# Performance work log

Measured on AMD Instinct MI355X. Metric: run time of the kernel, lower is better.

Reference implementation:

```python
import jax, jax.numpy as jnp
import numpy as np
from jax import lax

V, EMB, ENH, DNH, ZD, K = 51, 64, 256, 256, 32, 512
B, T = 1024, 128


def gru_scan(xs, h0, Wih, Whh, bih, bhh, collect):
    """PyTorch-convention GRU. xs: [T,B,D], h0: [B,H]. Returns (ys or None, hT)."""
    def step(h, x):
        gi = x @ Wih.T + bih          # [B, 3H]
        gh = h @ Whh.T + bhh          # [B, 3H]
        ir, iz, inn = jnp.split(gi, 3, axis=-1)
        hr, hz, hn = jnp.split(gh, 3, axis=-1)
        r = jax.nn.sigmoid(ir + hr)
        zg = jax.nn.sigmoid(iz + hz)
        n = jnp.tanh(inn + r * hn)
        hnew = (1.0 - zg) * n + zg * h
        return hnew, (hnew if collect else None)
    hT, ys = lax.scan(step, h0, xs)
    return ys, hT


def setup_inputs() -> dict:
    key = jax.random.key(0)
    ks = jax.random.split(key, 24)
    w = lambda k, shape, s=0.1: (jax.random.normal(k, shape, jnp.float32) * s)
    inp = {
        "x": jax.random.randint(ks[0], (B, T), 0, V),
        "emb_enc": w(ks[1], (V, EMB)),
        "emb_dec": w(ks[2], (V, EMB)),
        # encoder bidirectional GRU (fwd + bwd directions)
        "Wih_f": w(ks[3], (3 * ENH, EMB)), "Whh_f": w(ks[4], (3 * ENH, ENH)),
        "bih_f": w(ks[5], (3 * ENH,)), "bhh_f": w(ks[6], (3 * ENH,)),
        "Wih_b": w(ks[7], (3 * ENH, EMB)), "Whh_b": w(ks[8], (3 * ENH, ENH)),
        "bih_b": w(ks[9], (3 * ENH,)), "bhh_b": w(ks[10], (3 * ENH,)),
        # down_to_z: Linear(2*ENC_NH -> Z_NH)
        "Wdown": w(ks[11], (ZD, 2 * ENH)), "bdown": w(ks[12], (ZD,)),
        # VQ codebook, uniform(-1/K, 1/K) as in source
        "codebook": jax.random.uniform(ks[13], (K, ZD), jnp.float32, -1.0 / K, 1.0 / K),
        # up_from_z: Linear(Z_NH -> DEC_NH)
        "Wup": w(ks[14], (DNH, ZD)), "bup": w(ks[15], (DNH,)),
        # decoder GRU: input = INPUT_EMB_DIM + Z_NH
        "Wih_d": w(ks[16], (3 * DNH, EMB + ZD)), "Whh_d": w(ks[17], (3 * DNH, DNH)),
        "bih_d": w(ks[18], (3 * DNH,)), "bhh_d": w(ks[19], (3 * DNH,)),
        # output projection Linear(DEC_NH -> VOCABSIZE)
        "Wout": w(ks[20], (V, DNH)), "bout": w(ks[21], (V,)),
    }
    return inp


def reference(x, emb_enc, emb_dec, Wih_f, Whh_f, bih_f, bhh_f,
              Wih_b, Whh_b, bih_b, bhh_b, Wdown, bdown, codebook,
              Wup, bup, Wih_d, Whh_d, bih_d, bhh_d, Wout, bout):
    sg = lax.stop_gradient
    Bsz, Tlen = x.shape

    # ---- Encoder: bidirectional GRU, keep final hidden of each direction ----
    e = emb_enc[x]                              # [B,T,EMB]
    xs = jnp.transpose(e, (1, 0, 2))            # [T,B,EMB]
    h0 = jnp.zeros((Bsz, ENH), e.dtype)
    _, hf = gru_scan(xs, h0, Wih_f, Whh_f, bih_f, bhh_f, collect=False)
    _, hb = gru_scan(xs[::-1], h0, Wih_b, Whh_b, bih_b, bhh_b, collect=False)
    out_h = jnp.concatenate([hf, hb], axis=-1)  # [B, 2*ENH]

    # ---- down to z ----
    z = out_h @ Wdown.T + bdown                 # [B, ZD]

    # ---- VQ quantizer ----
    d2 = (z ** 2).sum(-1, keepdims=True) + (codebook ** 2).sum(-1) - 2.0 * (z @ codebook.T)  # [B,K]
    idx = jnp.argmin(d2, axis=-1)               # [B]
    quantized = codebook[idx]                   # [B, ZD]
    commit = ((sg(quantized) - z) ** 2).mean(-1)
    embed_l = ((quantized - sg(z)) ** 2).mean(-1)
    qloss = 0.1 * commit + 0.1 * embed_l
    Q = jnp.sum(qloss)
    qz = z + sg(quantized - z)                  # straight-through [B, ZD]

    # ---- up to decoder hidden ----
    hidden = qz @ Wup.T + bup                   # [B, DNH]

    # ---- Decoder GRU over src, z concatenated at every step ----
    src, tgt = x[:, :-1], x[:, 1:]
    d = emb_dec[src]                            # [B,T-1,EMB]
    zrep = jnp.broadcast_to(qz[:, None, :], (Bsz, Tlen - 1, ZD))
    dec_in = jnp.concatenate([zrep, d], axis=-1)            # [B,T-1,EMB+ZD]
    ys, _ = gru_scan(jnp.transpose(dec_in, (1, 0, 2)), hidden,
                     Wih_d, Whh_d, bih_d, bhh_d, collect=True)  # [T-1,B,DNH]
    logits = jnp.transpose(ys, (1, 0, 2)) @ Wout.T + bout   # [B,T-1,V]

    # cross entropy, reduction='sum', ignore_index=0
    logp = jax.nn.log_softmax(logits, axis=-1)
    nll = -jnp.take_along_axis(logp, tgt[..., None], axis=-1).squeeze(-1)  # [B,T-1]
    mask = (tgt != 0)
    xloss = jnp.sum(nll * mask)
    nonpadded_tokens = jnp.sum(mask)
    pred_tokens = jnp.argmax(logits, axis=-1)

    return (xloss, nonpadded_tokens, pred_tokens, Q, idx[:, None])
```

## Files before the change

kernel.cpp:

```cpp
#include <hip/hip_runtime.h>
#include <cstdint>

typedef unsigned short u16;
typedef unsigned int u32;
typedef __attribute__((ext_vector_type(4))) int int4v;
typedef __attribute__((ext_vector_type(8))) short short8;
typedef __attribute__((ext_vector_type(4))) float f32x4;

#define XLOSS_OFF 0
#define NPAD_OFF  1
#define PRED_OFF  2
#define Q_OFF     130050
#define IDX_OFF   130051

__device__ __forceinline__ u16 f2b(float f){
  union { float f; unsigned int i; } c; c.f = f;
  unsigned int i = c.i;
  unsigned int r = (i + 0x7FFFu + ((i >> 16) & 1u)) >> 16;
  return (u16)r;
}

#define LOG2E 1.442695040889634f
__device__ __forceinline__ float fast_sigmoid(float x){
  return __builtin_amdgcn_rcpf(1.f + __builtin_amdgcn_exp2f(-LOG2E*x));
}
__device__ __forceinline__ float fast_tanh(float x){
  return 1.f - 2.f*__builtin_amdgcn_rcpf(1.f + __builtin_amdgcn_exp2f((2.f*LOG2E)*x));
}

__global__ __launch_bounds__(256) void k_prep_wo(
    const float* __restrict__ Wo, u16* __restrict__ oWo, float* __restrict__ dout){
  int idx = blockIdx.x*256 + threadIdx.x;
  if (idx == 0){ dout[XLOSS_OFF]=0.f; dout[NPAD_OFF]=0.f; dout[Q_OFF]=0.f; }
  int row = idx >> 8, k = idx & 255;
  oWo[idx] = (row < 51) ? f2b(Wo[row*256 + k]) : (u16)0;
}

__global__ __launch_bounds__(64) void k_prep_q(
    const float* __restrict__ Wf, const float* __restrict__ Wb, const float* __restrict__ Wd,
    signed char* __restrict__ qf, signed char* __restrict__ qb, signed char* __restrict__ qd,
    float* __restrict__ invf, float* __restrict__ invb, float* __restrict__ invd){
  const int row = blockIdx.x;
  const int mat = row / 768, r = row - mat*768;
  const float* W = (mat==0 ? Wf : (mat==1 ? Wb : Wd)) + (size_t)r*256;
  signed char* q = (mat==0 ? qf : (mat==1 ? qb : qd)) + (size_t)r*256;
  float* inv     = (mat==0 ? invf : (mat==1 ? invb : invd));
  const int lane = threadIdx.x;
  float4 v = *(const float4*)(W + lane*4);
  float m = fmaxf(fmaxf(fabsf(v.x),fabsf(v.y)), fmaxf(fabsf(v.z),fabsf(v.w)));
  #pragma unroll
  for (int off=32; off>0; off>>=1) m = fmaxf(m, __shfl_xor(m, off));
  m = fmaxf(m, 1e-20f);
  const float s = 127.f / m;
  int a0 = __float2int_rn(v.x*s), a1 = __float2int_rn(v.y*s);
  int a2 = __float2int_rn(v.z*s), a3 = __float2int_rn(v.w*s);
  u32 packed = (a0&255) | ((a1&255)<<8) | ((a2&255)<<16) | ((a3&255)<<24);
  *(u32*)(q + lane*4) = packed;
  if (lane == 0) inv[r] = m * (1.f/127.f);
}

__global__ __launch_bounds__(256) void k_prep_g(
    const float* __restrict__ emb_e, const float* __restrict__ emb_d,
    const float* __restrict__ Wih_f, const float* __restrict__ bih_f, const float* __restrict__ bhh_f,
    const float* __restrict__ Wih_b, const float* __restrict__ bih_b, const float* __restrict__ bhh_b,
    const float* __restrict__ Wih_d,
    float* __restrict__ Gf, float* __restrict__ Gb, float* __restrict__ Gd){
  int idx = blockIdx.x*256 + threadIdx.x;
  int tab = idx / 39168;
  int rem = idx - tab*39168;
  int v = rem / 768;
  int n = rem - v*768;
  float acc = 0.f;
  if (tab == 0){
    const float* e = emb_e + v*64; const float* w = Wih_f + n*64;
    for (int k=0;k<64;k++) acc += e[k]*w[k];
    acc += bih_f[n] + (n < 512 ? bhh_f[n] : 0.f);
    Gf[rem] = acc;
  } else if (tab == 1){
    const float* e = emb_e + v*64; const float* w = Wih_b + n*64;
    for (int k=0;k<64;k++) acc += e[k]*w[k];
    acc += bih_b[n] + (n < 512 ? bhh_b[n] : 0.f);
    Gb[rem] = acc;
  } else {
    const float* e = emb_d + v*64; const float* w = Wih_d + n*96 + 32;
    for (int k=0;k<64;k++) acc += e[k]*w[k];
    Gd[rem] = acc;
  }
}

template<int MODE>
__global__ __launch_bounds__(512)
__attribute__((amdgpu_waves_per_eu(2, 2)))
void k_gru(
    const signed char* __restrict__ W0, const signed char* __restrict__ W1,
    const float* __restrict__ I0, const float* __restrict__ I1,
    const float* __restrict__ G0, const float* __restrict__ G1,
    const float* __restrict__ bhh0, const float* __restrict__ bhh1,
    const int* __restrict__ x,
    const float* __restrict__ zc, const float* __restrict__ h0g,
    float* __restrict__ out_h, u16* __restrict__ ys){
  __shared__ signed char hbf[2*4096];
  __shared__ int xsh[2048];

  const int tid = threadIdx.x;
  const int lane = tid & 63;
  const int wave = tid >> 6;
  const int l15 = lane & 15, lhi = lane >> 4;

  bool fwd = true; int gb;
  const signed char* W; const float* G; const float* bhh; const float* invS;
  if (MODE == 0){
    int bi = blockIdx.x;
    fwd = bi < 64; gb = fwd ? bi : bi - 64;
    W = fwd ? W0 : W1; G = fwd ? G0 : G1; bhh = fwd ? bhh0 : bhh1;
    invS = fwd ? I0 : I1;
  } else {
    gb = blockIdx.x; W = W0; G = G0; bhh = bhh0; invS = I0;
  }
  const int b0 = gb * 16;
  const int nT = (MODE == 0) ? 128 : 127;
  const float HS    = (MODE == 0) ? 127.f : 63.f;
  const float invHS = (MODE == 0) ? (1.f/127.f) : (1.f/63.f);

  const int ca  = wave*32 + l15;
  const int cb2 = ca + 16;

  int4v wq[6][4];
  #pragma unroll
  for (int g=0; g<3; g++){
    #pragma unroll
    for (int hh=0; hh<2; hh++){
      const signed char* p = W + (size_t)(g*256 + wave*32 + hh*16 + l15)*256 + lhi*16;
      #pragma unroll
      for (int kt=0; kt<4; kt++)
        wq[g*2+hh][kt] = *(const int4v*)(p + kt*64);
    }
  }
  #pragma unroll
  for (int kt=0; kt<4; kt++){
    asm volatile("" : "+v"(wq[0][kt]));
    asm volatile("" : "+v"(wq[1][kt]));
    asm volatile("" : "+v"(wq[2][kt]));
    asm volatile("" : "+v"(wq[3][kt]));
    asm volatile("" : "+v"(wq[4][kt]));
    asm volatile("" : "+v"(wq[5][kt]));
  }
  const float is0 = invS[ca]        * invHS;
  const float is1 = invS[cb2]       * invHS;
  const float is2 = invS[256 + ca]  * invHS;
  const float is3 = invS[256 + cb2] * invHS;
  const float is4 = invS[512 + ca]  * invHS;
  const float is5 = invS[512 + cb2] * invHS;
  const float bn0 = bhh[512 + ca];
  const float bn1 = bhh[512 + cb2];

  for (int i = tid; i < 2048; i += 512) xsh[i] = x[b0*128 + i];

  float hr0[4], hr1[4];
  #pragma unroll
  for (int r=0;r<4;r++){
    const int m = 4*lhi + r;
    const int sw = (m&15)<<4;
    float v0 = (MODE==0) ? 0.f : h0g[(size_t)(b0+m)*256 + ca];
    float v1 = (MODE==0) ? 0.f : h0g[(size_t)(b0+m)*256 + cb2];
    hr0[r] = v0; hr1[r] = v1;
    int q0 = __float2int_rn(fminf(fmaxf(v0*HS, -127.f), 127.f));
    int q1 = __float2int_rn(fminf(fmaxf(v1*HS, -127.f), 127.f));
    hbf[m*256 + (ca  ^ sw)] = (signed char)q0;
    hbf[m*256 + (cb2 ^ sw)] = (signed char)q1;
  }
  __syncthreads();

  int aoff[4];
  #pragma unroll
  for (int kt=0; kt<4; kt++)
    aoff[kt] = l15*256 + ((kt*64 + lhi*16) ^ (l15<<4));

  int cur = 0;
  for (int t=0; t<nT; ++t){
    const signed char* hb = hbf + (cur<<12);
    int4v af[4];
    #pragma unroll
    for (int kt=0; kt<4; kt++) af[kt] = *(const int4v*)(hb + aoff[kt]);

    int4v acc[6];
    #pragma unroll
    for (int j=0;j<6;j++) acc[j] = (int4v){0,0,0,0};
    #pragma unroll
    for (int kt=0; kt<4; kt++)
      #pragma unroll
      for (int j=0;j<6;j++)
        acc[j] = __builtin_amdgcn_mfma_i32_16x16x64_i8(af[kt], wq[j][kt], acc[j], 0,0,0);

    const int te = (MODE==0 && !fwd) ? (127 - t) : t;
    signed char* nbuf = hbf + ((cur^1)<<12);
    #pragma unroll
    for (int r=0;r<4;r++){
      const int m = 4*lhi + r;
      const int tok = xsh[(m<<7) + te];
      const float* Gp = G + (size_t)tok*768;
      float gr0 = Gp[ca],  gz0 = Gp[256+ca],  gn0 = Gp[512+ca];
      float gr1 = Gp[cb2], gz1 = Gp[256+cb2], gn1 = Gp[512+cb2];
      if (MODE==1){
        const float* zp = zc + (size_t)(b0+m)*768;
        gr0 += zp[ca];  gz0 += zp[256+ca];  gn0 += zp[512+ca];
        gr1 += zp[cb2]; gz1 += zp[256+cb2]; gn1 += zp[512+cb2];
      }
      const int sw = (m&15)<<4;
      {
        float rg = fast_sigmoid((float)acc[0][r]*is0 + gr0);
        float zg = fast_sigmoid((float)acc[2][r]*is2 + gz0);
        float nn = fast_tanh(gn0 + rg*((float)acc[4][r]*is4 + bn0));
        float hv = nn + zg*(hr0[r] - nn);
        hr0[r] = hv;
        int hq = __float2int_rn(fminf(fmaxf(hv*HS, -127.f), 127.f));
        nbuf[m*256 + (ca ^ sw)] = (signed char)hq;
        if (MODE == 1) ys[((size_t)(b0+m)*127 + t)*256 + ca] = f2b(hv);
      }
      {
        float rg = fast_sigmoid((float)acc[1][r]*is1 + gr1);
        float zg = fast_sigmoid((float)acc[3][r]*is3 + gz1);
        float nn = fast_tanh(gn1 + rg*((float)acc[5][r]*is5 + bn1));
        float hv = nn + zg*(hr1[r] - nn);
        hr1[r] = hv;
        int hq = __float2int_rn(fminf(fmaxf(hv*HS, -127.f), 127.f));
        nbuf[m*256 + (cb2 ^ sw)] = (signed char)hq;
        if (MODE == 1) ys[((size_t)(b0+m)*127 + t)*256 + cb2] = f2b(hv);
      }
    }
    __syncthreads();
    cur ^= 1;
  }

  if (MODE == 0){
    #pragma unroll
    for (int r=0;r<4;r++){
      const int m = 4*lhi + r;
      float* dst = out_h + (size_t)(b0+m)*512 + (fwd ? 0 : 256);
      dst[ca]  = hr0[r];
      dst[cb2] = hr1[r];
    }
  }
}

__global__ __launch_bounds__(64) void k_vq(
    const float* __restrict__ outH, const float* __restrict__ Wdown, const float* __restrict__ bdown,
    const float* __restrict__ cb, const float* __restrict__ Wup, const float* __restrict__ bup,
    const float* __restrict__ Wihd, const float* __restrict__ bihd, const float* __restrict__ bhhd,
    float* __restrict__ hidden, float* __restrict__ zc, float* __restrict__ dout){
  const int b = blockIdx.x;
  const int lane = threadIdx.x;
  __shared__ float oh[512];
  __shared__ float zsh[32];
  __shared__ float qsh[32];
  {
    const float* src = outH + (size_t)b*512 + lane*8;
    *(float4*)&oh[lane*8]   = *(const float4*)src;
    *(float4*)&oh[lane*8+4] = *(const float4*)(src+4);
  }
  __syncthreads();
  if (lane < 32){
    float acc = bdown[lane];
    const float* wr = Wdown + lane*512;
    for (int k=0;k<512;k++) acc += wr[k]*oh[k];
    zsh[lane] = acc;
  }
  __syncthreads();
  float bd = 3.4e38f; int bi = 0;
  for (int c8=0;c8<8;c8++){
    const int c = lane*8 + c8;
    const float* cr = cb + c*32;
    float d = 0.f;
    #pragma unroll
    for (int k=0;k<32;k++){ float df = zsh[k]-cr[k]; d += df*df; }
    if (d < bd){ bd = d; bi = c; }
  }
  #pragma unroll
  for (int offm=32; offm>0; offm>>=1){
    float od = __shfl_xor(bd, offm);
    int   oi = __shfl_xor(bi, offm);
    if (od < bd || (od == bd && oi < bi)){ bd = od; bi = oi; }
  }
  if (lane == 0){
    atomicAdd(&dout[Q_OFF], bd * (0.2f/32.f));
    dout[IDX_OFF + b] = (float)bi;
  }
  if (lane < 32) qsh[lane] = cb[(size_t)bi*32 + lane];
  __syncthreads();
  #pragma unroll
  for (int i=0;i<4;i++){
    const int o = lane*4 + i;
    float acc = bup[o];
    const float* wr = Wup + o*32;
    #pragma unroll
    for (int k=0;k<32;k++) acc += wr[k]*qsh[k];
    hidden[(size_t)b*256 + o] = acc;
  }
  #pragma unroll
  for (int i=0;i<12;i++){
    const int o = lane*12 + i;
    float acc = bihd[o] + (o < 512 ? bhhd[o] : 0.f);
    const float* wr = Wihd + (size_t)o*96;
    #pragma unroll
    for (int k=0;k<32;k++) acc += wr[k]*qsh[k];
    zc[(size_t)b*768 + o] = acc;
  }
}

__global__ __launch_bounds__(256) void k_out(
    const u16* __restrict__ ys, const u16* __restrict__ Wo,
    const float* __restrict__ bout, const int* __restrict__ x,
    float* __restrict__ dout){
  const int tid = threadIdx.x;
  const int w = tid >> 6, lane = tid & 63;
  const int l15 = lane & 15, lhi = lane >> 4;
  __shared__ float lg[4][32][66];
  const int rows0 = blockIdx.x*128 + w*32;
  const f32x4 fz = {0.f,0.f,0.f,0.f};
  #pragma unroll
  for (int mt=0; mt<2; mt++){
    const int rb = rows0 + mt*16;
    f32x4 acc[4];
    #pragma unroll
    for (int nt=0;nt<4;nt++) acc[nt] = fz;
    #pragma unroll
    for (int kt=0; kt<8; kt++){
      short8 a = *(const short8*)&ys[(size_t)(rb + l15)*256 + kt*32 + lhi*8];
      #pragma unroll
      for (int nt=0; nt<4; nt++){
        short8 bb = *(const short8*)&Wo[(size_t)(nt*16 + l15)*256 + kt*32 + lhi*8];
        acc[nt] = __builtin_amdgcn_mfma_f32_16x16x32_bf16(a, bb, acc[nt], 0, 0, 0);
      }
    }
    #pragma unroll
    for (int nt=0;nt<4;nt++){
      const int col = nt*16 + l15;
      const float bo = (col < 51) ? bout[col] : 0.f;
      #pragma unroll
      for (int r=0;r<4;r++){
        float v = (col < 51) ? (acc[nt][r] + bo) : -1e30f;
        lg[w][mt*16 + lhi*4 + r][col] = v;
      }
    }
  }
  __syncthreads();
  float xl = 0.f, ct = 0.f;
  if (lane < 32){
    const int grow = rows0 + lane;
    const float* Lr = &lg[w][lane][0];
    float m = Lr[0]; int am = 0;
    for (int i=1;i<51;i++){ float v = Lr[i]; if (v > m){ m = v; am = i; } }
    float s = 0.f;
    for (int i=0;i<51;i++) s += __expf(Lr[i] - m);
    const int bb = grow / 127;
    const int tt = grow - bb*127;
    const int tgt = x[bb*128 + tt + 1];
    const float nll = (m + __logf(s)) - Lr[tgt];
    const float mk = (tgt != 0) ? 1.f : 0.f;
    dout[PRED_OFF + grow] = (float)am;
    xl = nll * mk; ct = mk;
  }
  #pragma unroll
  for (int off=32; off>0; off>>=1){
    xl += __shfl_xor(xl, off);
    ct += __shfl_xor(ct, off);
  }
  if (lane == 0){
    atomicAdd(&dout[XLOSS_OFF], xl);
    atomicAdd(&dout[NPAD_OFF], ct);
  }
}

extern "C" void kernel_launch(void* const* d_in, const int* in_sizes, int n_in,
                              void* d_out, int out_size, void* d_ws, size_t ws_size,
                              hipStream_t stream){
  (void)in_sizes; (void)n_in; (void)out_size; (void)ws_size;
  const int*   x      = (const int*)  d_in[0];
  const float* emb_e  = (const float*)d_in[1];
  const float* emb_d  = (const float*)d_in[2];
  const float* Wih_f  = (const float*)d_in[3];
  const float* Whh_f  = (const float*)d_in[4];
  const float* bih_f  = (const float*)d_in[5];
  const float* bhh_f  = (const float*)d_in[6];
  const float* Wih_b  = (const float*)d_in[7];
  const float* Whh_b  = (const float*)d_in[8];
  const float* bih_b  = (const float*)d_in[9];
  const float* bhh_b  = (const float*)d_in[10];
  const float* Wdown  = (const float*)d_in[11];
  const float* bdown  = (const float*)d_in[12];
  const float* cbook  = (const float*)d_in[13];
  const float* Wup    = (const float*)d_in[14];
  const float* bup    = (const float*)d_in[15];
  const float* Wih_d  = (const float*)d_in[16];
  const float* Whh_d  = (const float*)d_in[17];
  const float* bih_d  = (const float*)d_in[18];
  const float* bhh_d  = (const float*)d_in[19];
  const float* Wout   = (const float*)d_in[20];
  const float* bout   = (const float*)d_in[21];
  float* dout = (float*)d_out;

  char* ws = (char*)d_ws;
  size_t off = 0;
  auto nxt = [&](size_t bytes)->char*{
    char* r = ws + off;
    off += (bytes + 255) & ~(size_t)255;
    return r;
  };
  signed char* Wq_f = (signed char*)nxt((size_t)196608);
  signed char* Wq_b = (signed char*)nxt((size_t)196608);
  signed char* Wq_d = (signed char*)nxt((size_t)196608);
  float* invF = (float*)nxt((size_t)768*4);
  float* invB = (float*)nxt((size_t)768*4);
  float* invD = (float*)nxt((size_t)768*4);
  float* Gf    = (float*)nxt((size_t)39168*4);
  float* Gb    = (float*)nxt((size_t)39168*4);
  float* Gd    = (float*)nxt((size_t)39168*4);
  u16*   Wo_bf = (u16*) nxt((size_t)16384*2);
  float* outH  = (float*)nxt((size_t)524288*4);
  float* hid   = (float*)nxt((size_t)262144*4);
  float* zcw   = (float*)nxt((size_t)786432*4);
  u16*   ysb   = (u16*)  nxt((size_t)33292288*2);

  hipLaunchKernelGGL(k_prep_wo, dim3(64), dim3(256), 0, stream, Wout, Wo_bf, dout);
  hipLaunchKernelGGL(k_prep_q, dim3(2304), dim3(64), 0, stream,
                     Whh_f, Whh_b, Whh_d, Wq_f, Wq_b, Wq_d, invF, invB, invD);
  hipLaunchKernelGGL(k_prep_g, dim3(459), dim3(256), 0, stream,
                     emb_e, emb_d, Wih_f, bih_f, bhh_f, Wih_b, bih_b, bhh_b, Wih_d,
                     Gf, Gb, Gd);
  hipLaunchKernelGGL((k_gru<0>), dim3(128), dim3(512), 0, stream,
                     Wq_f, Wq_b, invF, invB, Gf, Gb, bhh_f, bhh_b, x,
                     (const float*)nullptr, (const float*)nullptr, outH, (u16*)nullptr);
  hipLaunchKernelGGL(k_vq, dim3(1024), dim3(64), 0, stream,
                     outH, Wdown, bdown, cbook, Wup, bup, Wih_d, bih_d, bhh_d,
                     hid, zcw, dout);
  hipLaunchKernelGGL((k_gru<1>), dim3(64), dim3(512), 0, stream,
                     Wq_d, (const signed char*)nullptr, invD, (const float*)nullptr,
                     Gd, (const float*)nullptr, bhh_d, (const float*)nullptr, x,
                     zcw, hid, (float*)nullptr, ysb);
  hipLaunchKernelGGL(k_out, dim3(1016), dim3(256), 0, stream,
                     ysb, Wo_bf, bout, x, dout);
}
```

Baseline: 601.3 us.

## Halve GRU batch per block and redistribute gate math via LDS

Each GRU block now handles 8 batch rows instead of 16, doubling the grid so more CUs take part in the sequential recurrence. The MFMA tiles still compute 16 rows, so half the work is padding. Accumulators are staged through shared memory, letting each wave handle one batch row with vectorised 4-wide gate math, packed int8 and bf16 stores, and a zc tile cached in LDS. The token-dependent G loads are issued before the MFMAs. In exchange each timestep gets an extra barrier and more LDS traffic.

```diff
diff --git a/kernel.cpp b/kernel.cpp
--- a/kernel.cpp
+++ b/kernel.cpp
@@ -100,7 +100,9 @@
     const float* __restrict__ zc, const float* __restrict__ h0g,
     float* __restrict__ out_h, u16* __restrict__ ys){
   __shared__ signed char hbf[2*4096];
-  __shared__ int xsh[2048];
+  __shared__ int xsh[1024];
+  __shared__ int gh[8*772];
+  __shared__ float zcs[(MODE==1) ? 8*768 : 4];
 
   const int tid = threadIdx.x;
   const int lane = tid & 63;
@@ -111,19 +113,16 @@
   const signed char* W; const float* G; const float* bhh; const float* invS;
   if (MODE == 0){
     int bi = blockIdx.x;
-    fwd = bi < 64; gb = fwd ? bi : bi - 64;
+    fwd = bi < 128; gb = fwd ? bi : bi - 128;
     W = fwd ? W0 : W1; G = fwd ? G0 : G1; bhh = fwd ? bhh0 : bhh1;
     invS = fwd ? I0 : I1;
   } else {
     gb = blockIdx.x; W = W0; G = G0; bhh = bhh0; invS = I0;
   }
-  const int b0 = gb * 16;
+  const int b0 = gb * 8;
   const int nT = (MODE == 0) ? 128 : 127;
   const float HS    = (MODE == 0) ? 127.f : 63.f;
   const float invHS = (MODE == 0) ? (1.f/127.f) : (1.f/63.f);
-
-  const int ca  = wave*32 + l15;
-  const int cb2 = ca + 16;
 
   int4v wq[6][4];
   #pragma unroll
@@ -145,29 +144,38 @@
     asm volatile("" : "+v"(wq[4][kt]));
     asm volatile("" : "+v"(wq[5][kt]));
   }
-  const float is0 = invS[ca]        * invHS;
-  const float is1 = invS[cb2]       * invHS;
-  const float is2 = invS[256 + ca]  * invHS;
-  const float is3 = invS[256 + cb2] * invHS;
-  const float is4 = invS[512 + ca]  * invHS;
-  const float is5 = invS[512 + cb2] * invHS;
-  const float bn0 = bhh[512 + ca];
-  const float bn1 = bhh[512 + cb2];
-
-  for (int i = tid; i < 2048; i += 512) xsh[i] = x[b0*128 + i];
-
-  float hr0[4], hr1[4];
-  #pragma unroll
-  for (int r=0;r<4;r++){
-    const int m = 4*lhi + r;
-    const int sw = (m&15)<<4;
-    float v0 = (MODE==0) ? 0.f : h0g[(size_t)(b0+m)*256 + ca];
-    float v1 = (MODE==0) ? 0.f : h0g[(size_t)(b0+m)*256 + cb2];
-    hr0[r] = v0; hr1[r] = v1;
-    int q0 = __float2int_rn(fminf(fmaxf(v0*HS, -127.f), 127.f));
-    int q1 = __float2int_rn(fminf(fmaxf(v1*HS, -127.f), 127.f));
-    hbf[m*256 + (ca  ^ sw)] = (signed char)q0;
-    hbf[m*256 + (cb2 ^ sw)] = (signed char)q1;
+
+  const int gm = wave;
+  const int c4 = lane * 4;
+  f32x4 isr4 = *(const f32x4*)(invS + c4);
+  f32x4 isz4 = *(const f32x4*)(invS + 256 + c4);
+  f32x4 isn4 = *(const f32x4*)(invS + 512 + c4);
+  #pragma unroll
+  for (int i=0;i<4;i++){ isr4[i] *= invHS; isz4[i] *= invHS; isn4[i] *= invHS; }
+  const f32x4 bn4 = *(const f32x4*)(bhh + 512 + c4);
+
+  for (int i = tid; i < 1024; i += 512) xsh[i] = x[b0*128 + i];
+  for (int i = tid*4; i < 8192; i += 2048) *(int*)&hbf[i] = 0;
+  if (MODE == 1){
+    const f32x4* src = (const f32x4*)(zc + (size_t)b0*768);
+    f32x4* dst = (f32x4*)zcs;
+    for (int i = tid; i < 1536; i += 512) dst[i] = src[i];
+  }
+  __syncthreads();
+
+  float hreg[4];
+  #pragma unroll
+  for (int i=0;i<4;i++) hreg[i] = 0.f;
+  if (MODE == 1){
+    f32x4 h0v = *(const f32x4*)(h0g + (size_t)(b0+gm)*256 + c4);
+    u32 pk = 0;
+    #pragma unroll
+    for (int i=0;i<4;i++){
+      hreg[i] = h0v[i];
+      int q = __float2int_rn(fminf(fmaxf(h0v[i]*HS, -127.f), 127.f));
+      pk |= (u32)(q & 255) << (8*i);
+    }
+    *(u32*)&hbf[gm*256 + (c4 ^ (gm<<4))] = pk;
   }
   __syncthreads();
 
@@ -178,6 +186,13 @@
 
   int cur = 0;
   for (int t=0; t<nT; ++t){
+    const int te = (MODE==0 && !fwd) ? (127 - t) : t;
+    const int tok = xsh[(gm<<7) + te];
+    const float* Gp = G + (size_t)tok*768 + c4;
+    f32x4 gr4 = *(const f32x4*)(Gp);
+    f32x4 gz4 = *(const f32x4*)(Gp + 256);
+    f32x4 gn4 = *(const f32x4*)(Gp + 512);
+
     const signed char* hb = hbf + (cur<<12);
     int4v af[4];
     #pragma unroll
@@ -192,54 +207,55 @@
       for (int j=0;j<6;j++)
         acc[j] = __builtin_amdgcn_mfma_i32_16x16x64_i8(af[kt], wq[j][kt], acc[j], 0,0,0);
 
-    const int te = (MODE==0 && !fwd) ? (127 - t) : t;
-    signed char* nbuf = hbf + ((cur^1)<<12);
-    #pragma unroll
-    for (int r=0;r<4;r++){
-      const int m = 4*lhi + r;
-      const int tok = xsh[(m<<7) + te];
-      const float* Gp = G + (size_t)tok*768;
-      float gr0 = Gp[ca],  gz0 = Gp[256+ca],  gn0 = Gp[512+ca];
-      float gr1 = Gp[cb2], gz1 = Gp[256+cb2], gn1 = Gp[512+cb2];
-      if (MODE==1){
-        const float* zp = zc + (size_t)(b0+m)*768;
-        gr0 += zp[ca];  gz0 += zp[256+ca];  gn0 += zp[512+ca];
-        gr1 += zp[cb2]; gz1 += zp[256+cb2]; gn1 += zp[512+cb2];
+    if (lhi < 2){
+      #pragma unroll
+      for (int j=0;j<6;j++){
+        const int g = j >> 1;
+        const int col = wave*32 + (j&1)*16 + l15;
+        #pragma unroll
+        for (int r=0;r<4;r++)
+          gh[(4*lhi+r)*772 + g*256 + col] = acc[j][r];
       }
-      const int sw = (m&15)<<4;
-      {
-        float rg = fast_sigmoid((float)acc[0][r]*is0 + gr0);
-        float zg = fast_sigmoid((float)acc[2][r]*is2 + gz0);
-        float nn = fast_tanh(gn0 + rg*((float)acc[4][r]*is4 + bn0));
-        float hv = nn + zg*(hr0[r] - nn);
-        hr0[r] = hv;
-        int hq = __float2int_rn(fminf(fmaxf(hv*HS, -127.f), 127.f));
-        nbuf[m*256 + (ca ^ sw)] = (signed char)hq;
-        if (MODE == 1) ys[((size_t)(b0+m)*127 + t)*256 + ca] = f2b(hv);
-      }
-      {
-        float rg = fast_sigmoid((float)acc[1][r]*is1 + gr1);
-        float zg = fast_sigmoid((float)acc[3][r]*is3 + gz1);
-        float nn = fast_tanh(gn1 + rg*((float)acc[5][r]*is5 + bn1));
-        float hv = nn + zg*(hr1[r] - nn);
-        hr1[r] = hv;
-        int hq = __float2int_rn(fminf(fmaxf(hv*HS, -127.f), 127.f));
-        nbuf[m*256 + (cb2 ^ sw)] = (signed char)hq;
-        if (MODE == 1) ys[((size_t)(b0+m)*127 + t)*256 + cb2] = f2b(hv);
-      }
+    }
+    __syncthreads();
+
+    int4v hiR = *(const int4v*)&gh[gm*772 + c4];
+    int4v hiZ = *(const int4v*)&gh[gm*772 + 256 + c4];
+    int4v hiN = *(const int4v*)&gh[gm*772 + 512 + c4];
+    f32x4 zr4 = {0.f,0.f,0.f,0.f}, zz4 = zr4, zn4 = zr4;
+    if (MODE == 1){
+      zr4 = *(const f32x4*)&zcs[gm*768 + c4];
+      zz4 = *(const f32x4*)&zcs[gm*768 + 256 + c4];
+      zn4 = *(const f32x4*)&zcs[gm*768 + 512 + c4];
+    }
+    u32 pk = 0;
+    #pragma unroll
+    for (int i=0;i<4;i++){
+      float gr = gr4[i] + zr4[i];
+      float gz = gz4[i] + zz4[i];
+      float gn = gn4[i] + zn4[i];
+      float rg = fast_sigmoid((float)hiR[i]*isr4[i] + gr);
+      float zg = fast_sigmoid((float)hiZ[i]*isz4[i] + gz);
+      float nn = fast_tanh(gn + rg*((float)hiN[i]*isn4[i] + bn4[i]));
+      float hv = nn + zg*(hreg[i] - nn);
+      hreg[i] = hv;
+      int q = __float2int_rn(fminf(fmaxf(hv*HS, -127.f), 127.f));
+      pk |= (u32)(q & 255) << (8*i);
+    }
+    *(u32*)&hbf[((cur^1)<<12) + gm*256 + (c4 ^ (gm<<4))] = pk;
+    if (MODE == 1){
+      u32 lo = (u32)f2b(hreg[0]) | ((u32)f2b(hreg[1]) << 16);
+      u32 hi = (u32)f2b(hreg[2]) | ((u32)f2b(hreg[3]) << 16);
+      uint2 v; v.x = lo; v.y = hi;
+      *(uint2*)&ys[((size_t)(b0+gm)*127 + t)*256 + c4] = v;
     }
     __syncthreads();
     cur ^= 1;
   }
 
   if (MODE == 0){
-    #pragma unroll
-    for (int r=0;r<4;r++){
-      const int m = 4*lhi + r;
-      float* dst = out_h + (size_t)(b0+m)*512 + (fwd ? 0 : 256);
-      dst[ca]  = hr0[r];
-      dst[cb2] = hr1[r];
-    }
+    f32x4 o = {hreg[0], hreg[1], hreg[2], hreg[3]};
+    *(f32x4*)(out_h + (size_t)(b0+gm)*512 + (fwd ? 0 : 256) + c4) = o;
   }
 }
 
@@ -427,13 +443,13 @@
   hipLaunchKernelGGL(k_prep_g, dim3(459), dim3(256), 0, stream,
                      emb_e, emb_d, Wih_f, bih_f, bhh_f, Wih_b, bih_b, bhh_b, Wih_d,
                      Gf, Gb, Gd);
-  hipLaunchKernelGGL((k_gru<0>), dim3(128), dim3(512), 0, stream,
+  hipLaunchKernelGGL((k_gru<0>), dim3(256), dim3(512), 0, stream,
                      Wq_f, Wq_b, invF, invB, Gf, Gb, bhh_f, bhh_b, x,
                      (const float*)nullptr, (const float*)nullptr, outH, (u16*)nullptr);
   hipLaunchKernelGGL(k_vq, dim3(1024), dim3(64), 0, stream,
                      outH, Wdown, bdown, cbook, Wup, bup, Wih_d, bih_d, bhh_d,
                      hid, zcw, dout);
-  hipLaunchKernelGGL((k_gru<1>), dim3(64), dim3(512), 0, stream,
+  hipLaunchKernelGGL((k_gru<1>), dim3(128), dim3(512), 0, stream,
                      Wq_d, (const signed char*)nullptr, invD, (const float*)nullptr,
                      Gd, (const float*)nullptr, bhh_d, (const float*)nullptr, x,
                      zcw, hid, (float*)nullptr, ysb);
```

Result: faster. 531.6 us (-11.6%).
